# Kernel optimization log

Measured on AMD Instinct MI355X. Metric: run time of the kernel, lower is better.

The kernel has to match this reference:

```python
import jax, jax.numpy as jnp
import numpy as np
import math

KEY_DIM = 16
COMPAT_FACTOR = 1.0 / math.sqrt(KEY_DIM)


def setup_inputs() -> dict:
    key = jax.random.key(0)
    k1, k2, k3, k4, k5 = jax.random.split(key, 5)
    B, G, D, H, K, V = 4, 2048, 128, 8, 16, 16
    h = jax.random.normal(k1, (B, G, D), dtype=jnp.float32)
    # mask: 1 = masked-out (attention forced to zero), 0 = attend
    mask = jax.random.randint(k2, (G, G), 0, 2, dtype=jnp.int32)
    # xavier_uniform over (input_dim, key_dim) fan per head
    lim_qk = math.sqrt(6.0 / (D + K))
    lim_v = math.sqrt(6.0 / (D + V))
    W_Q = jax.random.uniform(k3, (H, D, K), jnp.float32, -lim_qk, lim_qk)
    W_K = jax.random.uniform(k4, (H, D, K), jnp.float32, -lim_qk, lim_qk)
    W_V = jax.random.uniform(k5, (H, D, V), jnp.float32, -lim_v, lim_v)
    return {"h": h, "mask": mask, "W_Q": W_Q, "W_K": W_K, "W_V": W_V}


def reference(h, mask, W_Q, W_K, W_V):
    # h: [B, G, D]; W_Q/W_K: [H, D, K]; W_V: [H, D, V]; mask: [G, G] (1 = masked)
    q = jnp.einsum("bgd,hdk->bhgk", h, W_Q)  # [B, H, G, K]
    k = jnp.einsum("bgd,hdk->bhgk", h, W_K)  # [B, H, G, K]
    v = jnp.einsum("bgd,hdv->bhgv", h, W_V)  # [B, H, G, V]
    compat = COMPAT_FACTOR * jnp.einsum("bhqk,bhgk->bhqg", q, k)  # [B, H, G, G]
    masked = (mask > 0)[None, None, :, :]  # broadcast over batch, heads
    neg = jnp.finfo(compat.dtype).min
    compat = jnp.where(masked, neg, compat)
    attn = jax.nn.softmax(compat, axis=-1)
    # post-softmax hard zeroing at masked positions (as in the original)
    attn = jnp.where(masked, jnp.zeros((), attn.dtype), attn)
    h_p = jnp.einsum("bhqg,bhgv->bhqv", attn, v)  # [B, H, G, V]
    return h_p
```

## Files before the change

kernel.cpp:

```cpp
#include <hip/hip_runtime.h>
#include <hip/hip_bf16.h>

#define GG 2048
#define DD 128
#define HH 8
#define BH 32

typedef _Float16 h2 __attribute__((ext_vector_type(2)));
typedef _Float16 h4 __attribute__((ext_vector_type(4)));
typedef _Float16 h8 __attribute__((ext_vector_type(8)));
typedef __attribute__((ext_vector_type(4))) float f32x4;
typedef unsigned short u16;
typedef unsigned int   u32;
typedef unsigned char  u8;
typedef unsigned long long u64;

#define QSCALE 0.36067376022224085f

#define OFF_Q  0u
#define OFF_KV (2u << 20)
#define OFF_M  (6u << 20)

#if __has_builtin(__builtin_amdgcn_exp2f)
#define EXP2F(x) __builtin_amdgcn_exp2f(x)
#else
#define EXP2F(x) exp2f(x)
#endif

#define MFMA16(a, b, c) __builtin_amdgcn_mfma_f32_16x16x16f16(a, b, c, 0, 0, 0)

static __device__ __forceinline__ u16 f16b(float x) {
  return __builtin_bit_cast(u16, (_Float16)x);
}

__global__ __launch_bounds__(256) void prep_kernel(
    const float* __restrict__ h, const int* __restrict__ mask,
    const float* __restrict__ WQ, const float* __restrict__ WK,
    const float* __restrict__ WV,
    _Float16* __restrict__ Qh, u8* __restrict__ KVp, u8* __restrict__ mbt)
{
  const int blk = blockIdx.x, tid = threadIdx.x;

  if (blk >= 256) {
    int t = (blk - 256) * 256 + tid;
    const int* m = mask + (size_t)t * 8;
    int4 m0 = *(const int4*)m;
    int4 m1 = *(const int4*)(m + 4);
    u32 byte = (m0.x > 0) | ((m0.y > 0) << 1) | ((m0.z > 0) << 2) | ((m0.w > 0) << 3)
             | ((m1.x > 0) << 4) | ((m1.y > 0) << 5) | ((m1.z > 0) << 6) | ((m1.w > 0) << 7);
    int q  = t >> 8;
    int k8 = t & 255;
    mbt[(size_t)(k8 >> 4) * (GG * 16) + (size_t)q * 16 + (k8 & 15)] = (u8)byte;
    return;
  }

  __shared__ _Float16 Wl[48 * 136];
  const int bh = blk >> 3, b = bh >> 3, hh = bh & (HH - 1);

  #pragma unroll
  for (int m = 0; m < 3; ++m) {
    const float* W = (m == 0 ? WQ : (m == 1 ? WK : WV)) + (size_t)hh * DD * 16;
    const float sc = (m == 0) ? QSCALE : 1.0f;
    #pragma unroll
    for (int i = 0; i < 2; ++i) {
      int j4 = i * 256 + tid;
      float4 v = ((const float4*)W)[j4];
      int j = j4 * 4, d = j >> 4, n0 = m * 16 + (j & 15);
      Wl[(n0 + 0) * 136 + d] = (_Float16)(v.x * sc);
      Wl[(n0 + 1) * 136 + d] = (_Float16)(v.y * sc);
      Wl[(n0 + 2) * 136 + d] = (_Float16)(v.z * sc);
      Wl[(n0 + 3) * 136 + d] = (_Float16)(v.w * sc);
    }
  }
  __syncthreads();

  const int wave = tid >> 6, lane = tid & 63;
  const int col = lane & 15, quad = lane >> 4;
  const int g0 = ((blk & 7) * 4 + wave) * 64;
  const float* hb = h + (size_t)b * GG * DD;

  f32x4 acc[4][3];
  #pragma unroll
  for (int mt = 0; mt < 4; ++mt)
    #pragma unroll
    for (int nt = 0; nt < 3; ++nt)
      acc[mt][nt] = (f32x4){0.f, 0.f, 0.f, 0.f};

  #pragma unroll
  for (int s = 0; s < 4; ++s) {
    h8 a[4], bw[3];
    #pragma unroll
    for (int mt = 0; mt < 4; ++mt) {
      const float* src = hb + (size_t)(g0 + mt * 16 + col) * DD + s * 32 + quad * 8;
      float4 x = ((const float4*)src)[0];
      float4 y = ((const float4*)src)[1];
      a[mt] = (h8){ (_Float16)x.x, (_Float16)x.y, (_Float16)x.z, (_Float16)x.w,
                    (_Float16)y.x, (_Float16)y.y, (_Float16)y.z, (_Float16)y.w };
    }
    #pragma unroll
    for (int nt = 0; nt < 3; ++nt)
      bw[nt] = *(const h8*)&Wl[(nt * 16 + col) * 136 + s * 32 + quad * 8];
    #pragma unroll
    for (int mt = 0; mt < 4; ++mt)
      #pragma unroll
      for (int nt = 0; nt < 3; ++nt)
        acc[mt][nt] = __builtin_amdgcn_mfma_f32_16x16x32_f16(a[mt], bw[nt], acc[mt][nt], 0, 0, 0);
  }

  u8* kvb = KVp + (size_t)bh * 16 * 8192;
  #pragma unroll
  for (int mt = 0; mt < 4; ++mt) {
    #pragma unroll
    for (int r = 0; r < 4; ++r) {
      int g = g0 + mt * 16 + quad * 4 + r;
      Qh[((size_t)bh * GG + g) * 16 + col] = (_Float16)acc[mt][0][r];
      int gi = g & 127;
      u8* tb = kvb + (size_t)(g >> 7) * 8192;
      *(u16*)(tb + gi * 32 + col * 2) = f16b(acc[mt][1][r]);
      *(u16*)(tb + 4096 + col * 256 + ((((gi >> 2) + col) & 31) * 8)
                 + (g & 3) * 2) = f16b(acc[mt][2][r]);
    }
  }
}

__global__ __launch_bounds__(512, 4) void attn_kernel(
    const _Float16* __restrict__ Qh, const u8* __restrict__ KVp,
    const u8* __restrict__ mbt, float* __restrict__ out)
{
  __shared__ __align__(16) u8 kv[2][16384];
  __shared__ float Lacc[8][16][17];
  __shared__ float Ll[8][16];
  __shared__ __align__(16) f32x4 cmLUT[16];
  const int tid = threadIdx.x, wv = tid >> 6, lane = tid & 63;
  const int col = lane & 15, quad = lane >> 4;
  const int qp = wv & 3;
  const int kh = wv >> 2;
  const int bh = blockIdx.x & 31;
  const int qt0 = qp * 2, qt1 = qp * 2 + 1;
  const int qb0 = (blockIdx.x >> 5) * 128 + qt0 * 16;
  const int qb1 = qb0 + 16;

  if (tid < 16) {
    f32x4 e;
    e[0] = (tid & 1) ? -3000.f : -4.f;
    e[1] = (tid & 2) ? -3000.f : -4.f;
    e[2] = (tid & 4) ? -3000.f : -4.f;
    e[3] = (tid & 8) ? -3000.f : -4.f;
    cmLUT[tid] = e;
  }

  const h4 qf0 = *(const h4*)(Qh + ((size_t)bh * GG + qb0 + col) * 16 + quad * 4);
  const h4 qf1 = *(const h4*)(Qh + ((size_t)bh * GG + qb1 + col) * 16 + quad * 4);
  const u8* kvsrc = KVp + (size_t)bh * 16 * 8192;
  const u8* mrow0 = mbt + (size_t)(qb0 + col) * 16;
  const u8* mrow1 = mbt + (size_t)(qb1 + col) * 16;

  f32x4 acc0 = {0.f,0.f,0.f,0.f}, lacc0 = {0.f,0.f,0.f,0.f};
  f32x4 acc1 = {0.f,0.f,0.f,0.f}, lacc1 = {0.f,0.f,0.f,0.f};
  const h4 ones = {(_Float16)1.f, (_Float16)1.f, (_Float16)1.f, (_Float16)1.f};
  const int shq = quad * 4;

  int voff[8];
  #pragma unroll
  for (int st = 0; st < 8; ++st)
    voff[st] = kh * 8192 + 4096 + col * 256 + (((st * 4 + quad + col) & 31) * 8);
  const int koff = kh * 8192;

  const int sh2 = tid >> 8, stid = tid & 255;

  {
    const u8* src = kvsrc + (size_t)(sh2 * 8) * 8192;
    *(uint4*)(kv[0] + sh2 * 8192 + stid * 16)        = *(const uint4*)(src + stid * 16);
    *(uint4*)(kv[0] + sh2 * 8192 + 4096 + stid * 16) = *(const uint4*)(src + 4096 + stid * 16);
  }
  const size_t tstep = (size_t)(GG * 16);
  uint4 mv0 = *(const uint4*)(mrow0 + (size_t)(kh * 8) * tstep);
  uint4 mv1 = *(const uint4*)(mrow1 + (size_t)(kh * 8) * tstep);
  __syncthreads();

  for (int it = 0; it < 8; ++it) {
    uint4 ns0, ns1, nm0, nm1;
    if (it < 7) {
      const u8* src = kvsrc + (size_t)(sh2 * 8 + it + 1) * 8192;
      ns0 = *(const uint4*)(src + stid * 16);
      ns1 = *(const uint4*)(src + 4096 + stid * 16);
      nm0 = *(const uint4*)(mrow0 + (size_t)(kh * 8 + it + 1) * tstep);
      nm1 = *(const uint4*)(mrow1 + (size_t)(kh * 8 + it + 1) * tstep);
    }

    const u8* cur = kv[it & 1];
    const _Float16* ldsK = (const _Float16*)(cur + koff);
    u64 a0 = ((u64)mv0.x | ((u64)mv0.y << 32)) >> shq;
    u64 a1 = ((u64)mv0.z | ((u64)mv0.w << 32)) >> shq;
    u64 b0 = ((u64)mv1.x | ((u64)mv1.y << 32)) >> shq;
    u64 b1 = ((u64)mv1.z | ((u64)mv1.w << 32)) >> shq;

    #pragma unroll
    for (int st = 0; st < 8; ++st) {
      h4 kf = *(const h4*)(ldsK + (size_t)(st * 16 + col) * 16 + quad * 4);
      h4 vf = *(const h4*)(cur + voff[st]);

      u32 bitsA = (u32)(((st < 4) ? a0 : a1) >> ((st & 3) * 16)) & 0xFu;
      u32 bitsB = (u32)(((st < 4) ? b0 : b1) >> ((st & 3) * 16)) & 0xFu;
      const f32x4 cmA = cmLUT[bitsA];
      const f32x4 cmB = cmLUT[bitsB];

      f32x4 s0 = MFMA16(kf, qf0, cmA);
      f32x4 s1 = MFMA16(kf, qf1, cmB);
      float p0 = EXP2F(s0[0]);
      float p1 = EXP2F(s0[1]);
      float p2 = EXP2F(s0[2]);
      float p3 = EXP2F(s0[3]);
      float r0 = EXP2F(s1[0]);
      float r1 = EXP2F(s1[1]);
      float r2 = EXP2F(s1[2]);
      float r3 = EXP2F(s1[3]);

      h2 a01 = __builtin_bit_cast(h2, __builtin_amdgcn_cvt_pkrtz(p0, p1));
      h2 a23 = __builtin_bit_cast(h2, __builtin_amdgcn_cvt_pkrtz(p2, p3));
      h4 pf0 = __builtin_shufflevector(a01, a23, 0, 1, 2, 3);
      h2 c01 = __builtin_bit_cast(h2, __builtin_amdgcn_cvt_pkrtz(r0, r1));
      h2 c23 = __builtin_bit_cast(h2, __builtin_amdgcn_cvt_pkrtz(r2, r3));
      h4 pf1 = __builtin_shufflevector(c01, c23, 0, 1, 2, 3);

      acc0  = MFMA16(vf, pf0, acc0);
      acc1  = MFMA16(vf, pf1, acc1);
      lacc0 = MFMA16(ones, pf0, lacc0);
      lacc1 = MFMA16(ones, pf1, lacc1);
    }

    if (it < 7) {
      u8* dst = kv[(it + 1) & 1] + sh2 * 8192;
      *(uint4*)(dst + stid * 16)        = ns0;
      *(uint4*)(dst + 4096 + stid * 16) = ns1;
      mv0 = nm0; mv1 = nm1;
      __syncthreads();
    }
  }

  const float l0 = lacc0[0], l1 = lacc1[0];
  if (kh == 0) {
    #pragma unroll
    for (int r = 0; r < 4; ++r) {
      Lacc[qt0][col][shq + r] = acc0[r];
      Lacc[qt1][col][shq + r] = acc1[r];
    }
    if (quad == 0) { Ll[qt0][col] = l0; Ll[qt1][col] = l1; }
  }
  __syncthreads();
  if (kh == 1) {
    float la0 = Ll[qt0][col] + l0;
    float ra0 = (la0 > 0.f) ? (1.f / la0) : 0.f;
    float4 o0;
    o0.x = (Lacc[qt0][col][shq + 0] + acc0[0]) * ra0;
    o0.y = (Lacc[qt0][col][shq + 1] + acc0[1]) * ra0;
    o0.z = (Lacc[qt0][col][shq + 2] + acc0[2]) * ra0;
    o0.w = (Lacc[qt0][col][shq + 3] + acc0[3]) * ra0;
    *(float4*)(out + ((size_t)bh * GG + qb0 + col) * 16 + shq) = o0;

    float la1 = Ll[qt1][col] + l1;
    float ra1 = (la1 > 0.f) ? (1.f / la1) : 0.f;
    float4 o1;
    o1.x = (Lacc[qt1][col][shq + 0] + acc1[0]) * ra1;
    o1.y = (Lacc[qt1][col][shq + 1] + acc1[1]) * ra1;
    o1.z = (Lacc[qt1][col][shq + 2] + acc1[2]) * ra1;
    o1.w = (Lacc[qt1][col][shq + 3] + acc1[3]) * ra1;
    *(float4*)(out + ((size_t)bh * GG + qb1 + col) * 16 + shq) = o1;
  }
}

extern "C" void kernel_launch(void* const* d_in, const int* in_sizes, int n_in,
                              void* d_out, int out_size, void* d_ws, size_t ws_size,
                              hipStream_t stream) {
  const float* h    = (const float*)d_in[0];
  const int*   mask = (const int*)d_in[1];
  const float* WQ   = (const float*)d_in[2];
  const float* WK   = (const float*)d_in[3];
  const float* WV   = (const float*)d_in[4];
  float* out = (float*)d_out;
  char* ws = (char*)d_ws;
  _Float16* Qh  = (_Float16*)(ws + OFF_Q);
  u8*       KVp = (u8*)(ws + OFF_KV);
  u8*       mbt = (u8*)(ws + OFF_M);

  hipLaunchKernelGGL(prep_kernel, dim3(256 + GG * GG / (256 * 8)), dim3(256), 0, stream,
                     h, mask, WQ, WK, WV, Qh, KVp, mbt);
  hipLaunchKernelGGL(attn_kernel, dim3(BH * (GG / 128)), dim3(512), 0, stream,
                     Qh, KVp, mbt, out);
}
```

Before: 103.3 us.

## Stage two KV tiles per barrier and coalesce mask bit-packing reads

The attention loop now double-buffers pairs of KV tiles, loading two 8KB tiles per stage. This halves the number of __syncthreads barriers and issues more global loads ahead of compute. LDS use doubles to 64KB for the KV buffers, and registers rise from holding four uint4 prefetches, which may lower occupancy under the 512-thread, 4-block launch bound. Separately, the mask-packing part of prep now maps threads so that each block writes a contiguous 16x16-byte tile, making the transposed bitmask stores more coalesced.

```diff
diff --git a/kernel.cpp b/kernel.cpp
--- a/kernel.cpp
+++ b/kernel.cpp
@@ -42,15 +42,17 @@
   const int blk = blockIdx.x, tid = threadIdx.x;
 
   if (blk >= 256) {
-    int t = (blk - 256) * 256 + tid;
-    const int* m = mask + (size_t)t * 8;
+    int blk2 = blk - 256;
+    int q0 = (blk2 >> 4) * 16;
+    int g8 = blk2 & 15;
+    int qq = tid >> 4, kk = tid & 15;
+    int q = q0 + qq;
+    const int* m = mask + (size_t)q * GG + (size_t)(g8 * 16 + kk) * 8;
     int4 m0 = *(const int4*)m;
     int4 m1 = *(const int4*)(m + 4);
     u32 byte = (m0.x > 0) | ((m0.y > 0) << 1) | ((m0.z > 0) << 2) | ((m0.w > 0) << 3)
              | ((m1.x > 0) << 4) | ((m1.y > 0) << 5) | ((m1.z > 0) << 6) | ((m1.w > 0) << 7);
-    int q  = t >> 8;
-    int k8 = t & 255;
-    mbt[(size_t)(k8 >> 4) * (GG * 16) + (size_t)q * 16 + (k8 & 15)] = (u8)byte;
+    mbt[(size_t)g8 * (GG * 16) + (size_t)q * 16 + kk] = (u8)byte;
     return;
   }
 
@@ -127,7 +129,7 @@
     const _Float16* __restrict__ Qh, const u8* __restrict__ KVp,
     const u8* __restrict__ mbt, float* __restrict__ out)
 {
-  __shared__ __align__(16) u8 kv[2][16384];
+  __shared__ __align__(16) u8 kv[2][2][16384];
   __shared__ float Lacc[8][16][17];
   __shared__ float Ll[8][16];
   __shared__ __align__(16) f32x4 cmLUT[16];
@@ -169,71 +171,90 @@
   const int sh2 = tid >> 8, stid = tid & 255;
 
   {
-    const u8* src = kvsrc + (size_t)(sh2 * 8) * 8192;
-    *(uint4*)(kv[0] + sh2 * 8192 + stid * 16)        = *(const uint4*)(src + stid * 16);
-    *(uint4*)(kv[0] + sh2 * 8192 + 4096 + stid * 16) = *(const uint4*)(src + 4096 + stid * 16);
+    const u8* s0 = kvsrc + (size_t)(sh2 * 8 + 0) * 8192;
+    const u8* s1 = kvsrc + (size_t)(sh2 * 8 + 1) * 8192;
+    *(uint4*)(kv[0][0] + sh2 * 8192 + stid * 16)        = *(const uint4*)(s0 + stid * 16);
+    *(uint4*)(kv[0][0] + sh2 * 8192 + 4096 + stid * 16) = *(const uint4*)(s0 + 4096 + stid * 16);
+    *(uint4*)(kv[0][1] + sh2 * 8192 + stid * 16)        = *(const uint4*)(s1 + stid * 16);
+    *(uint4*)(kv[0][1] + sh2 * 8192 + 4096 + stid * 16) = *(const uint4*)(s1 + 4096 + stid * 16);
   }
   const size_t tstep = (size_t)(GG * 16);
   uint4 mv0 = *(const uint4*)(mrow0 + (size_t)(kh * 8) * tstep);
   uint4 mv1 = *(const uint4*)(mrow1 + (size_t)(kh * 8) * tstep);
   __syncthreads();
 
-  for (int it = 0; it < 8; ++it) {
-    uint4 ns0, ns1, nm0, nm1;
-    if (it < 7) {
-      const u8* src = kvsrc + (size_t)(sh2 * 8 + it + 1) * 8192;
-      ns0 = *(const uint4*)(src + stid * 16);
-      ns1 = *(const uint4*)(src + 4096 + stid * 16);
-      nm0 = *(const uint4*)(mrow0 + (size_t)(kh * 8 + it + 1) * tstep);
-      nm1 = *(const uint4*)(mrow1 + (size_t)(kh * 8 + it + 1) * tstep);
-    }
-
-    const u8* cur = kv[it & 1];
-    const _Float16* ldsK = (const _Float16*)(cur + koff);
-    u64 a0 = ((u64)mv0.x | ((u64)mv0.y << 32)) >> shq;
-    u64 a1 = ((u64)mv0.z | ((u64)mv0.w << 32)) >> shq;
-    u64 b0 = ((u64)mv1.x | ((u64)mv1.y << 32)) >> shq;
-    u64 b1 = ((u64)mv1.z | ((u64)mv1.w << 32)) >> shq;
-
-    #pragma unroll
-    for (int st = 0; st < 8; ++st) {
-      h4 kf = *(const h4*)(ldsK + (size_t)(st * 16 + col) * 16 + quad * 4);
-      h4 vf = *(const h4*)(cur + voff[st]);
-
-      u32 bitsA = (u32)(((st < 4) ? a0 : a1) >> ((st & 3) * 16)) & 0xFu;
-      u32 bitsB = (u32)(((st < 4) ? b0 : b1) >> ((st & 3) * 16)) & 0xFu;
-      const f32x4 cmA = cmLUT[bitsA];
-      const f32x4 cmB = cmLUT[bitsB];
-
-      f32x4 s0 = MFMA16(kf, qf0, cmA);
-      f32x4 s1 = MFMA16(kf, qf1, cmB);
-      float p0 = EXP2F(s0[0]);
-      float p1 = EXP2F(s0[1]);
-      float p2 = EXP2F(s0[2]);
-      float p3 = EXP2F(s0[3]);
-      float r0 = EXP2F(s1[0]);
-      float r1 = EXP2F(s1[1]);
-      float r2 = EXP2F(s1[2]);
-      float r3 = EXP2F(s1[3]);
-
-      h2 a01 = __builtin_bit_cast(h2, __builtin_amdgcn_cvt_pkrtz(p0, p1));
-      h2 a23 = __builtin_bit_cast(h2, __builtin_amdgcn_cvt_pkrtz(p2, p3));
-      h4 pf0 = __builtin_shufflevector(a01, a23, 0, 1, 2, 3);
-      h2 c01 = __builtin_bit_cast(h2, __builtin_amdgcn_cvt_pkrtz(r0, r1));
-      h2 c23 = __builtin_bit_cast(h2, __builtin_amdgcn_cvt_pkrtz(r2, r3));
-      h4 pf1 = __builtin_shufflevector(c01, c23, 0, 1, 2, 3);
-
-      acc0  = MFMA16(vf, pf0, acc0);
-      acc1  = MFMA16(vf, pf1, acc1);
-      lacc0 = MFMA16(ones, pf0, lacc0);
-      lacc1 = MFMA16(ones, pf1, lacc1);
-    }
-
-    if (it < 7) {
-      u8* dst = kv[(it + 1) & 1] + sh2 * 8192;
-      *(uint4*)(dst + stid * 16)        = ns0;
-      *(uint4*)(dst + 4096 + stid * 16) = ns1;
-      mv0 = nm0; mv1 = nm1;
+  #pragma unroll
+  for (int p = 0; p < 4; ++p) {
+    uint4 nsA0, nsA1, nsB0, nsB1;
+    if (p < 3) {
+      const u8* sA = kvsrc + (size_t)(sh2 * 8 + 2 * p + 2) * 8192;
+      nsA0 = *(const uint4*)(sA + stid * 16);
+      nsA1 = *(const uint4*)(sA + 4096 + stid * 16);
+      const u8* sB = sA + 8192;
+      nsB0 = *(const uint4*)(sB + stid * 16);
+      nsB1 = *(const uint4*)(sB + 4096 + stid * 16);
+    }
+
+    #pragma unroll
+    for (int hh2 = 0; hh2 < 2; ++hh2) {
+      const int it = 2 * p + hh2;
+      uint4 nm0, nm1;
+      if (it < 7) {
+        nm0 = *(const uint4*)(mrow0 + (size_t)(kh * 8 + it + 1) * tstep);
+        nm1 = *(const uint4*)(mrow1 + (size_t)(kh * 8 + it + 1) * tstep);
+      }
+
+      const u8* cur = kv[p & 1][hh2];
+      const _Float16* ldsK = (const _Float16*)(cur + koff);
+      u64 a0 = ((u64)mv0.x | ((u64)mv0.y << 32)) >> shq;
+      u64 a1 = ((u64)mv0.z | ((u64)mv0.w << 32)) >> shq;
+      u64 b0 = ((u64)mv1.x | ((u64)mv1.y << 32)) >> shq;
+      u64 b1 = ((u64)mv1.z | ((u64)mv1.w << 32)) >> shq;
+
+      #pragma unroll
+      for (int st = 0; st < 8; ++st) {
+        h4 kf = *(const h4*)(ldsK + (size_t)(st * 16 + col) * 16 + quad * 4);
+        h4 vf = *(const h4*)(cur + voff[st]);
+
+        u32 bitsA = (u32)(((st < 4) ? a0 : a1) >> ((st & 3) * 16)) & 0xFu;
+        u32 bitsB = (u32)(((st < 4) ? b0 : b1) >> ((st & 3) * 16)) & 0xFu;
+        const f32x4 cmA = cmLUT[bitsA];
+        const f32x4 cmB = cmLUT[bitsB];
+
+        f32x4 s0 = MFMA16(kf, qf0, cmA);
+        f32x4 s1 = MFMA16(kf, qf1, cmB);
+        float p0 = EXP2F(s0[0]);
+        float p1 = EXP2F(s0[1]);
+        float p2 = EXP2F(s0[2]);
+        float p3 = EXP2F(s0[3]);
+        float r0 = EXP2F(s1[0]);
+        float r1 = EXP2F(s1[1]);
+        float r2 = EXP2F(s1[2]);
+        float r3 = EXP2F(s1[3]);
+
+        h2 a01 = __builtin_bit_cast(h2, __builtin_amdgcn_cvt_pkrtz(p0, p1));
+        h2 a23 = __builtin_bit_cast(h2, __builtin_amdgcn_cvt_pkrtz(p2, p3));
+        h4 pf0 = __builtin_shufflevector(a01, a23, 0, 1, 2, 3);
+        h2 c01 = __builtin_bit_cast(h2, __builtin_amdgcn_cvt_pkrtz(r0, r1));
+        h2 c23 = __builtin_bit_cast(h2, __builtin_amdgcn_cvt_pkrtz(r2, r3));
+        h4 pf1 = __builtin_shufflevector(c01, c23, 0, 1, 2, 3);
+
+        acc0  = MFMA16(vf, pf0, acc0);
+        acc1  = MFMA16(vf, pf1, acc1);
+        lacc0 = MFMA16(ones, pf0, lacc0);
+        lacc1 = MFMA16(ones, pf1, lacc1);
+      }
+
+      if (it < 7) { mv0 = nm0; mv1 = nm1; }
+    }
+
+    if (p < 3) {
+      u8* dA = kv[(p + 1) & 1][0] + sh2 * 8192;
+      *(uint4*)(dA + stid * 16)        = nsA0;
+      *(uint4*)(dA + 4096 + stid * 16) = nsA1;
+      u8* dB = kv[(p + 1) & 1][1] + sh2 * 8192;
+      *(uint4*)(dB + stid * 16)        = nsB0;
+      *(uint4*)(dB + 4096 + stid * 16) = nsB1;
       __syncthreads();
     }
   }
```

After: 101.8 us, median of 2. About the same (-1.5%).

## Load full per-head K/V into LDS once with 1024-thread blocks; tile mask packing

Applied to the files above, without the earlier changes.

The attention kernel now uses 1024-thread blocks covering 256 queries and loads the whole 128KB K/V slab for a head into LDS up front. This removes the double-buffered streaming loop and its per-iteration barriers, and halves the number of blocks that each re-read K/V. The mask packing in the prep kernel is retiled so each block handles 16 query rows by 16 key chunks, which changes its read and write access pattern. The cost is one block per CU with very large LDS use, an unoverlapped initial load, and half as many blocks across the GPU (256).

```diff
diff --git a/kernel.cpp b/kernel.cpp
--- a/kernel.cpp
+++ b/kernel.cpp
@@ -42,15 +42,17 @@
   const int blk = blockIdx.x, tid = threadIdx.x;
 
   if (blk >= 256) {
-    int t = (blk - 256) * 256 + tid;
-    const int* m = mask + (size_t)t * 8;
+    int blk2 = blk - 256;
+    int q0 = (blk2 >> 4) * 16;
+    int g8 = blk2 & 15;
+    int qq = tid >> 4, kk = tid & 15;
+    int q = q0 + qq;
+    const int* m = mask + (size_t)q * GG + (size_t)(g8 * 16 + kk) * 8;
     int4 m0 = *(const int4*)m;
     int4 m1 = *(const int4*)(m + 4);
     u32 byte = (m0.x > 0) | ((m0.y > 0) << 1) | ((m0.z > 0) << 2) | ((m0.w > 0) << 3)
              | ((m1.x > 0) << 4) | ((m1.y > 0) << 5) | ((m1.z > 0) << 6) | ((m1.w > 0) << 7);
-    int q  = t >> 8;
-    int k8 = t & 255;
-    mbt[(size_t)(k8 >> 4) * (GG * 16) + (size_t)q * 16 + (k8 & 15)] = (u8)byte;
+    mbt[(size_t)g8 * (GG * 16) + (size_t)q * 16 + kk] = (u8)byte;
     return;
   }
 
@@ -123,21 +125,21 @@
   }
 }
 
-__global__ __launch_bounds__(512, 4) void attn_kernel(
+__global__ __launch_bounds__(1024, 1) void attn_kernel(
     const _Float16* __restrict__ Qh, const u8* __restrict__ KVp,
     const u8* __restrict__ mbt, float* __restrict__ out)
 {
-  __shared__ __align__(16) u8 kv[2][16384];
-  __shared__ float Lacc[8][16][17];
-  __shared__ float Ll[8][16];
+  __shared__ __align__(16) u8 kv[16 * 8192];
+  __shared__ float Lacc[16][16][17];
+  __shared__ float Ll[16][16];
   __shared__ __align__(16) f32x4 cmLUT[16];
   const int tid = threadIdx.x, wv = tid >> 6, lane = tid & 63;
   const int col = lane & 15, quad = lane >> 4;
-  const int qp = wv & 3;
-  const int kh = wv >> 2;
+  const int qp = wv & 7;
+  const int kh = wv >> 3;
   const int bh = blockIdx.x & 31;
   const int qt0 = qp * 2, qt1 = qp * 2 + 1;
-  const int qb0 = (blockIdx.x >> 5) * 128 + qt0 * 16;
+  const int qb0 = (blockIdx.x >> 5) * 256 + qt0 * 16;
   const int qb1 = qb0 + 16;
 
   if (tid < 16) {
@@ -149,9 +151,14 @@
     cmLUT[tid] = e;
   }
 
+  const u8* kvsrc = KVp + (size_t)bh * 16 * 8192;
+  #pragma unroll
+  for (int r = 0; r < 8; ++r)
+    *(uint4*)(kv + (size_t)r * 16384 + tid * 16) =
+        *(const uint4*)(kvsrc + (size_t)r * 16384 + tid * 16);
+
   const h4 qf0 = *(const h4*)(Qh + ((size_t)bh * GG + qb0 + col) * 16 + quad * 4);
   const h4 qf1 = *(const h4*)(Qh + ((size_t)bh * GG + qb1 + col) * 16 + quad * 4);
-  const u8* kvsrc = KVp + (size_t)bh * 16 * 8192;
   const u8* mrow0 = mbt + (size_t)(qb0 + col) * 16;
   const u8* mrow1 = mbt + (size_t)(qb1 + col) * 16;
 
@@ -163,33 +170,23 @@
   int voff[8];
   #pragma unroll
   for (int st = 0; st < 8; ++st)
-    voff[st] = kh * 8192 + 4096 + col * 256 + (((st * 4 + quad + col) & 31) * 8);
-  const int koff = kh * 8192;
-
-  const int sh2 = tid >> 8, stid = tid & 255;
-
-  {
-    const u8* src = kvsrc + (size_t)(sh2 * 8) * 8192;
-    *(uint4*)(kv[0] + sh2 * 8192 + stid * 16)        = *(const uint4*)(src + stid * 16);
-    *(uint4*)(kv[0] + sh2 * 8192 + 4096 + stid * 16) = *(const uint4*)(src + 4096 + stid * 16);
-  }
+    voff[st] = 4096 + col * 256 + (((st * 4 + quad + col) & 31) * 8);
+
   const size_t tstep = (size_t)(GG * 16);
   uint4 mv0 = *(const uint4*)(mrow0 + (size_t)(kh * 8) * tstep);
   uint4 mv1 = *(const uint4*)(mrow1 + (size_t)(kh * 8) * tstep);
   __syncthreads();
 
+  #pragma unroll 2
   for (int it = 0; it < 8; ++it) {
-    uint4 ns0, ns1, nm0, nm1;
+    uint4 nm0, nm1;
     if (it < 7) {
-      const u8* src = kvsrc + (size_t)(sh2 * 8 + it + 1) * 8192;
-      ns0 = *(const uint4*)(src + stid * 16);
-      ns1 = *(const uint4*)(src + 4096 + stid * 16);
       nm0 = *(const uint4*)(mrow0 + (size_t)(kh * 8 + it + 1) * tstep);
       nm1 = *(const uint4*)(mrow1 + (size_t)(kh * 8 + it + 1) * tstep);
     }
 
-    const u8* cur = kv[it & 1];
-    const _Float16* ldsK = (const _Float16*)(cur + koff);
+    const u8* cur = kv + (size_t)(kh * 8 + it) * 8192;
+    const _Float16* ldsK = (const _Float16*)cur;
     u64 a0 = ((u64)mv0.x | ((u64)mv0.y << 32)) >> shq;
     u64 a1 = ((u64)mv0.z | ((u64)mv0.w << 32)) >> shq;
     u64 b0 = ((u64)mv1.x | ((u64)mv1.y << 32)) >> shq;
@@ -229,13 +226,7 @@
       lacc1 = MFMA16(ones, pf1, lacc1);
     }
 
-    if (it < 7) {
-      u8* dst = kv[(it + 1) & 1] + sh2 * 8192;
-      *(uint4*)(dst + stid * 16)        = ns0;
-      *(uint4*)(dst + 4096 + stid * 16) = ns1;
-      mv0 = nm0; mv1 = nm1;
-      __syncthreads();
-    }
+    if (it < 7) { mv0 = nm0; mv1 = nm1; }
   }
 
   const float l0 = lacc0[0], l1 = lacc1[0];
@@ -285,6 +276,6 @@
 
   hipLaunchKernelGGL(prep_kernel, dim3(256 + GG * GG / (256 * 8)), dim3(256), 0, stream,
                      h, mask, WQ, WK, WV, Qh, KVp, mbt);
-  hipLaunchKernelGGL(attn_kernel, dim3(BH * (GG / 128)), dim3(512), 0, stream,
+  hipLaunchKernelGGL(attn_kernel, dim3(BH * (GG / 256)), dim3(1024), 0, stream,
                      Qh, KVp, mbt, out);
 }
```

New measurement: 102.4 us. No clear change (-0.8%).
